# Optimization experiments

Hardware: AMD Instinct MI355X
Metric: run time of the kernel (lower is better)

The kernel has to match this reference:

```python
import jax, jax.numpy as jnp
import numpy as np

B, S, D = 8, 1024, 1024

def setup_inputs() -> dict:
    key = jax.random.key(0)
    ks = jax.random.split(key, 6)
    context = jax.random.normal(ks[0], (B, S, D), dtype=jnp.float32)
    eos_mask = jax.random.randint(ks[1], (B, S), 0, 2, dtype=jnp.int32)
    prior = jax.random.uniform(ks[2], (), dtype=jnp.float32)
    adj_mat = jax.random.randint(ks[3], (B, S, S), 0, 2, dtype=jnp.int32)
    Wk = jax.random.normal(ks[4], (D, D), dtype=jnp.float32) * 0.02
    Wq = jax.random.normal(ks[5], (D, D), dtype=jnp.float32) * 0.02
    bk = jnp.zeros((D,), jnp.float32)
    bq = jnp.zeros((D,), jnp.float32)
    ln_gamma = jnp.ones((D,), jnp.float32)
    ln_beta = jnp.zeros((D,), jnp.float32)
    return {"context": context, "eos_mask": eos_mask, "prior": prior,
            "adj_mat": adj_mat, "Wk": Wk, "bk": bk, "Wq": Wq, "bq": bq,
            "ln_gamma": ln_gamma, "ln_beta": ln_beta}

def reference(context, eos_mask, prior, adj_mat, Wk, bk, Wq, bq, ln_gamma, ln_beta):
    d_model = context.shape[-1]
    seq_len = context.shape[1]
    # LayerNorm (annotated-transformer style: unbiased std, eps added to std)
    mu = jnp.mean(context, axis=-1, keepdims=True)
    std = jnp.std(context, axis=-1, keepdims=True, ddof=1)
    x = ln_gamma * (context - mu) / (std + 1e-6) + ln_beta
    # projections (torch Linear: x @ W.T + b)
    key_p = x @ Wk.T + bk
    query = x @ Wq.T + bq
    scores = jnp.einsum('bqd,bkd->bqk', query, key_p) / (d_model / 2)
    scores = jnp.where(adj_mat == 0, -1e9, scores)
    neibor_attn = jax.nn.softmax(scores, axis=-1)
    neibor_attn = jnp.sqrt(neibor_attn * jnp.swapaxes(neibor_attn, -1, -2) + 1e-9)
    neibor_attn = prior + (1.0 - prior) * neibor_attn
    # constant structural matrices
    a = jnp.eye(seq_len, k=1, dtype=jnp.float32)          # superdiagonal
    b = jnp.eye(seq_len, dtype=jnp.float32)               # diagonal
    tri = jnp.triu(jnp.ones((seq_len, seq_len), jnp.float32))  # upper incl diag
    # t = (log(attn+eps) masked to superdiagonal) @ tri
    t = jnp.matmul(jnp.where(a == 0, 0.0, jnp.log(neibor_attn + 1e-9)), tri)
    g_attn = jnp.exp(jnp.matmul(tri, t))
    g_attn = jnp.where((tri - b) == 0, 0.0, g_attn)  # keep strict upper only
    g_attn = g_attn + jnp.swapaxes(g_attn, -1, -2) + jnp.where(b == 0, 1e-9, neibor_attn)
    return (g_attn, neibor_attn)
```

## Files before the change

kernel.cpp:

```cpp
#include <hip/hip_runtime.h>
#include <hip/hip_bf16.h>

#define S_LEN 1024
#define D_DIM 1024
#define N_BAT 8
#define BSS   (8ull*1024ull*1024ull)

using bf16x8 = __attribute__((ext_vector_type(8))) short;
using f32x4  = __attribute__((ext_vector_type(4))) float;

__device__ __forceinline__ short f2bf(float v) {
    __hip_bfloat16 h = __float2bfloat16(v);
    return *reinterpret_cast<short*>(&h);
}

__device__ __forceinline__ void gload_lds16(const void* g, void* l) {
    __builtin_amdgcn_global_load_lds(
        (const __attribute__((address_space(1))) void*)g,
        (__attribute__((address_space(3))) void*)l, 16, 0, 0);
}

__device__ __forceinline__ int xcd_remap_flat() {
    const int nwg  = gridDim.x * gridDim.y * gridDim.z;
    const int flat = blockIdx.x + gridDim.x * (blockIdx.y + gridDim.y * blockIdx.z);
    const int cpx  = nwg >> 3;
    return (flat & 7) * cpx + (flat >> 3);
}

__device__ __forceinline__ void gemm_mainloop(
    const short* __restrict__ A, const short* __restrict__ Bt,
    int brow, int bcol, short* As, short* Bs, f32x4 acc[4][4])
{
    const int tid  = threadIdx.x;
    const int lane = tid & 63;
    const int w    = tid >> 6;
    const int wr   = w >> 1, wc = w & 1;
    const int q0   = w * 4096 + lane * 16;
    const int rsel = lane & 15;
    const int kb   = (lane >> 4) * 16;

#pragma unroll
    for (int m = 0; m < 4; ++m)
#pragma unroll
        for (int n = 0; n < 4; ++n) acc[m][n] = 0.0f;

#pragma unroll
    for (int c = 0; c < 4; ++c) {
        const int q    = q0 + c * 1024;
        const int row  = q >> 7;
        const int colb = (q & 127) ^ ((row & 7) << 4);
        gload_lds16((const char*)(A  + (size_t)(brow + row) * 1024) + colb,
                    (char*)As + q);
        gload_lds16((const char*)(Bt + (size_t)(bcol + row) * 1024) + colb,
                    (char*)Bs + q);
    }
    __syncthreads();

    for (int t = 0; t < 16; ++t) {
        const int cur = t & 1;
        const char* Ac = (const char*)As + cur * 16384;
        const char* Bc = (const char*)Bs + cur * 16384;
        if (t < 15) {
            const int k0 = (t + 1) * 64;
            char* An = (char*)As + (cur ^ 1) * 16384;
            char* Bn = (char*)Bs + (cur ^ 1) * 16384;
#pragma unroll
            for (int c = 0; c < 4; ++c) {
                const int q    = q0 + c * 1024;
                const int row  = q >> 7;
                const int colb = (q & 127) ^ ((row & 7) << 4);
                gload_lds16((const char*)(A  + (size_t)(brow + row) * 1024 + k0) + colb,
                            An + q);
                gload_lds16((const char*)(Bt + (size_t)(bcol + row) * 1024 + k0) + colb,
                            Bn + q);
            }
        }
        bf16x8 af[4][2], bfr[4][2];
#pragma unroll
        for (int m = 0; m < 4; ++m) {
            const int row = wr * 64 + m * 16 + rsel;
            const int sw  = (row & 7) << 4;
#pragma unroll
            for (int kk = 0; kk < 2; ++kk)
                af[m][kk] = *(const bf16x8*)&Ac[row * 128 + ((kk * 64 + kb) ^ sw)];
        }
#pragma unroll
        for (int n = 0; n < 4; ++n) {
            const int row = wc * 64 + n * 16 + rsel;
            const int sw  = (row & 7) << 4;
#pragma unroll
            for (int kk = 0; kk < 2; ++kk)
                bfr[n][kk] = *(const bf16x8*)&Bc[row * 128 + ((kk * 64 + kb) ^ sw)];
        }
#pragma unroll
        for (int kk = 0; kk < 2; ++kk)
#pragma unroll
            for (int m = 0; m < 4; ++m)
#pragma unroll
                for (int n = 0; n < 4; ++n)
                    acc[m][n] = __builtin_amdgcn_mfma_f32_16x16x32_bf16(
                        af[m][kk], bfr[n][kk], acc[m][n], 0, 0, 0);
        __syncthreads();
    }
}

__global__ __launch_bounds__(256) void gemm_bf16(
    const short* __restrict__ A, const short* __restrict__ Bt,
    short* __restrict__ C)
{
    __shared__ short As[2 * 8192];
    __shared__ short Bs[2 * 8192];
    const int nid = xcd_remap_flat();
    const int mx  = nid % gridDim.x;
    const int ny  = nid / gridDim.x;
    const int brow = mx * 128, bcol = ny * 128;

    f32x4 acc[4][4];
    gemm_mainloop(A, Bt, brow, bcol, As, Bs, acc);

    const int lane = threadIdx.x & 63;
    const int w    = threadIdx.x >> 6;
    const int wr   = w >> 1, wc = w & 1;
#pragma unroll
    for (int m = 0; m < 4; ++m)
#pragma unroll
        for (int n = 0; n < 4; ++n) {
            const int colg = bcol + wc * 64 + n * 16 + (lane & 15);
#pragma unroll
            for (int r = 0; r < 4; ++r) {
                const int rowg = brow + wr * 64 + m * 16 + ((lane >> 4) * 4 + r);
                C[(size_t)rowg * 1024 + colg] = f2bf(acc[m][n][r]);
            }
        }
}

__global__ __launch_bounds__(256) void gemm_scores(
    const short* __restrict__ Tm, const short* __restrict__ Xm,
    const float* __restrict__ p, const float* __restrict__ r2,
    const float* __restrict__ c0p, float* __restrict__ Sc)
{
    __shared__ short As[2 * 8192];
    __shared__ short Bs[2 * 8192];
    const int nid = xcd_remap_flat();
    const int mx  = nid & 7;
    const int ny  = (nid >> 3) & 7;
    const int b   = nid >> 6;
    const short* A  = Tm + (size_t)b * 1024 * 1024;
    const short* Bt = Xm + (size_t)b * 1024 * 1024;
    const float* pb = p  + (size_t)b * 1024;
    const float* rb = r2 + (size_t)b * 1024;
    float* C = Sc + (size_t)b * 1024 * 1024;
    const int brow = mx * 128, bcol = ny * 128;

    f32x4 acc[4][4];
    gemm_mainloop(A, Bt, brow, bcol, As, Bs, acc);

    const int lane = threadIdx.x & 63;
    const int w    = threadIdx.x >> 6;
    const int wr   = w >> 1, wc = w & 1;
    const float c0v = c0p[0];
#pragma unroll
    for (int m = 0; m < 4; ++m)
#pragma unroll
        for (int n = 0; n < 4; ++n) {
            const int colg = bcol + wc * 64 + n * 16 + (lane & 15);
            const float radd = rb[colg] + c0v;
#pragma unroll
            for (int r = 0; r < 4; ++r) {
                const int rowg = brow + wr * 64 + m * 16 + ((lane >> 4) * 4 + r);
                C[(size_t)rowg * 1024 + colg] =
                    (acc[m][n][r] + pb[rowg] + radd) * 0.001953125f;
            }
        }
}

__global__ __launch_bounds__(256) void bias_gemv1(
    const float* __restrict__ Wq, const float* __restrict__ Wk,
    const float* __restrict__ bk, const float* __restrict__ bq,
    float* __restrict__ pu, float* __restrict__ pv)
{
    __shared__ float su[8][128];
    __shared__ float sv[8][128];
    const int tx = threadIdx.x & 31;
    const int ty = threadIdx.x >> 5;
    const int colBase = blockIdx.x * 128;
    const int rowBase = blockIdx.y * 64;
    const int i = colBase + tx * 4;
    float4 au = {0,0,0,0}, av = {0,0,0,0};
#pragma unroll
    for (int jj = 0; jj < 8; ++jj) {
        const int j = rowBase + ty + jj * 8;
        const float bkv = bk[j], bqv = bq[j];
        const float4 wq = *(const float4*)&Wq[(size_t)j * 1024 + i];
        const float4 wk = *(const float4*)&Wk[(size_t)j * 1024 + i];
        au.x += wq.x * bkv; au.y += wq.y * bkv; au.z += wq.z * bkv; au.w += wq.w * bkv;
        av.x += wk.x * bqv; av.y += wk.y * bqv; av.z += wk.z * bqv; av.w += wk.w * bqv;
    }
    ((float4*)su[ty])[tx] = au;
    ((float4*)sv[ty])[tx] = av;
    __syncthreads();
    if (ty == 0) {
        float4 s1 = ((float4*)su[0])[tx];
        float4 s2 = ((float4*)sv[0])[tx];
#pragma unroll
        for (int k = 1; k < 8; ++k) {
            const float4 t1 = ((float4*)su[k])[tx];
            const float4 t2 = ((float4*)sv[k])[tx];
            s1.x += t1.x; s1.y += t1.y; s1.z += t1.z; s1.w += t1.w;
            s2.x += t2.x; s2.y += t2.y; s2.z += t2.z; s2.w += t2.w;
        }
        ((float4*)&pu[(size_t)blockIdx.y * 1024 + colBase])[tx] = s1;
        ((float4*)&pv[(size_t)blockIdx.y * 1024 + colBase])[tx] = s2;
    }
}

__global__ __launch_bounds__(256) void bias_gemv2(
    const float* __restrict__ pu, const float* __restrict__ pv,
    const float* __restrict__ bk, const float* __restrict__ bq,
    float* __restrict__ u, float* __restrict__ v, float* __restrict__ c0)
{
    __shared__ float sh[4];
    const int i = blockIdx.x * 256 + threadIdx.x;
    float su = 0.0f, sv = 0.0f;
#pragma unroll
    for (int k = 0; k < 16; ++k) {
        su += pu[k * 1024 + i];
        sv += pv[k * 1024 + i];
    }
    u[i] = su;
    v[i] = sv;
    if (blockIdx.x == 0) {
        const int t = threadIdx.x;
        const float4 a = ((const float4*)bq)[t];
        const float4 b = ((const float4*)bk)[t];
        float s = a.x*b.x + a.y*b.y + a.z*b.z + a.w*b.w;
        for (int off = 32; off > 0; off >>= 1) s += __shfl_down(s, off);
        const int lane = t & 63, w = t >> 6;
        if (lane == 0) sh[w] = s;
        __syncthreads();
        if (t == 0) c0[0] = sh[0] + sh[1] + sh[2] + sh[3];
    }
}

__global__ __launch_bounds__(256) void ln_kernel(
    const float* __restrict__ X, const float* __restrict__ gamma,
    const float* __restrict__ beta, const float* __restrict__ u,
    const float* __restrict__ v2, short* __restrict__ Y,
    float* __restrict__ p, float* __restrict__ r2)
{
    __shared__ float sh[16];
    const size_t row = blockIdx.x;
    const int t = threadIdx.x;
    float4 v = ((const float4*)(X + row * 1024))[t];
    float s  = v.x + v.y + v.z + v.w;
    float ss = v.x*v.x + v.y*v.y + v.z*v.z + v.w*v.w;
    for (int off = 32; off > 0; off >>= 1) {
        s  += __shfl_down(s, off);
        ss += __shfl_down(ss, off);
    }
    const int lane = t & 63, w = t >> 6;
    if (lane == 0) { sh[w] = s; sh[4 + w] = ss; }
    __syncthreads();
    if (t == 0) {
        float S  = sh[0] + sh[1] + sh[2] + sh[3];
        float SS = sh[4] + sh[5] + sh[6] + sh[7];
        float mu = S * (1.0f / 1024.0f);
        float var = fmaxf((SS - S * mu) * (1.0f / 1023.0f), 0.0f);
        sh[0] = mu;
        sh[1] = 1.0f / (sqrtf(var) + 1e-6f);
    }
    __syncthreads();
    const float mu = sh[0], inv = sh[1];
    float4 g  = ((const float4*)gamma)[t];
    float4 be = ((const float4*)beta)[t];
    float y0 = g.x * (v.x - mu) * inv + be.x;
    float y1 = g.y * (v.y - mu) * inv + be.y;
    float y2 = g.z * (v.z - mu) * inv + be.z;
    float y3 = g.w * (v.w - mu) * inv + be.w;
    short4 o;
    o.x = f2bf(y0); o.y = f2bf(y1); o.z = f2bf(y2); o.w = f2bf(y3);
    ((short4*)(Y + row * 1024))[t] = o;
    float4 uu = ((const float4*)u)[t];
    float4 vv = ((const float4*)v2)[t];
    float dp = y0*uu.x + y1*uu.y + y2*uu.z + y3*uu.w;
    float dr = y0*vv.x + y1*vv.y + y2*vv.z + y3*vv.w;
    for (int off = 32; off > 0; off >>= 1) {
        dp += __shfl_down(dp, off);
        dr += __shfl_down(dr, off);
    }
    if (lane == 0) { sh[8 + w] = dp; sh[12 + w] = dr; }
    __syncthreads();
    if (t == 0) {
        p[row]  = sh[8] + sh[9] + sh[10] + sh[11];
        r2[row] = sh[12] + sh[13] + sh[14] + sh[15];
    }
}

__global__ __launch_bounds__(256) void cvt_t_kernel(
    const float* __restrict__ Wq, const float* __restrict__ Wk,
    short* __restrict__ wqt, short* __restrict__ wkt)
{
    __shared__ float T[32][33];
    const float* src = blockIdx.z ? Wk : Wq;
    short* dst = blockIdx.z ? wkt : wqt;
    const int bi = blockIdx.x * 32, bj = blockIdx.y * 32;
    const int c = threadIdx.x & 31, r0 = threadIdx.x >> 5;
#pragma unroll
    for (int rr = 0; rr < 4; ++rr) {
        const int r = r0 + rr * 8;
        T[r][c] = src[(size_t)(bi + r) * 1024 + bj + c];
    }
    __syncthreads();
#pragma unroll
    for (int rr = 0; rr < 4; ++rr) {
        const int r = r0 + rr * 8;
        dst[(size_t)(bj + r) * 1024 + bi + c] = f2bf(T[c][r]);
    }
}

__global__ __launch_bounds__(256) void softmax_kernel(
    const float* __restrict__ Sc, const int* __restrict__ adj,
    float* __restrict__ At)
{
    __shared__ float sh[4];
    const size_t row = blockIdx.x;
    const int t = threadIdx.x;
    const float4 sv = ((const float4*)(Sc + row * 1024))[t];
    const int4   av = ((const int4*)(adj + row * 1024))[t];
    float m = -3.0e38f;
    if (av.x) m = fmaxf(m, sv.x);
    if (av.y) m = fmaxf(m, sv.y);
    if (av.z) m = fmaxf(m, sv.z);
    if (av.w) m = fmaxf(m, sv.w);
    for (int off = 32; off > 0; off >>= 1) m = fmaxf(m, __shfl_down(m, off));
    const int lane = t & 63, w = t >> 6;
    if (lane == 0) sh[w] = m;
    __syncthreads();
    const float M = fmaxf(fmaxf(sh[0], sh[1]), fmaxf(sh[2], sh[3]));
    __syncthreads();
    float e0 = av.x ? expf(sv.x - M) : 0.0f;
    float e1 = av.y ? expf(sv.y - M) : 0.0f;
    float e2 = av.z ? expf(sv.z - M) : 0.0f;
    float e3 = av.w ? expf(sv.w - M) : 0.0f;
    float s = e0 + e1 + e2 + e3;
    for (int off = 32; off > 0; off >>= 1) s += __shfl_down(s, off);
    if (lane == 0) sh[w] = s;
    __syncthreads();
    const float Sm = sh[0] + sh[1] + sh[2] + sh[3];
    float4 o;
    if (Sm > 0.0f) {
        const float inv = 1.0f / Sm;
        o.x = e0 * inv; o.y = e1 * inv; o.z = e2 * inv; o.w = e3 * inv;
    } else {
        o.x = o.y = o.z = o.w = 1.0f / 1024.0f;
    }
    ((float4*)(At + row * 1024))[t] = o;
}

__global__ __launch_bounds__(1024) void cum2_kernel(
    const float* __restrict__ At, const float* __restrict__ prior_p,
    double* __restrict__ cum)
{
    __shared__ double sh[1024];
    const int b = blockIdx.x;
    const int t = threadIdx.x;
    const float prior = *prior_p;
    const float om = 1.0f - prior;
    const float* attn = At + (size_t)b * 1024 * 1024;
    double v = 0.0;
    if (t >= 1) {
        const int k = t - 1;
        const float a1 = attn[(size_t)k * 1024 + (k + 1)];
        const float a2 = attn[(size_t)(k + 1) * 1024 + k];
        const float na = prior + om * sqrtf(a1 * a2 + 1e-9f);
        v = (double)logf(na + 1e-9f);
    }
    sh[t] = v;
    __syncthreads();
#pragma unroll
    for (int off = 1; off < 1024; off <<= 1) {
        const double add = (t >= off) ? sh[t - off] : 0.0;
        __syncthreads();
        sh[t] += add;
        __syncthreads();
    }
    cum[b * 1024 + t] = sh[t];
}

__global__ __launch_bounds__(256) void na_g_kernel(
    float* __restrict__ At, const float* __restrict__ prior_p,
    const double* __restrict__ cum, float* __restrict__ G)
{
    const int ti = blockIdx.x >> 5, tj = blockIdx.x & 31;
    if (tj < ti) return;
    const int b = blockIdx.y;
    const float prior = *prior_p;
    const float om = 1.0f - prior;
    float* base = At + (size_t)b * 1024 * 1024;
    float* gb   = G  + (size_t)b * 1024 * 1024;
    const double* cb = cum + (size_t)b * 1024;
    __shared__ float T1[32][33];
    __shared__ float T2[32][33];
    const int c = threadIdx.x & 31, r0 = threadIdx.x >> 5;
#pragma unroll
    for (int rr = 0; rr < 4; ++rr) {
        const int r = r0 + rr * 8;
        T1[r][c] = base[(size_t)(ti * 32 + r) * 1024 + tj * 32 + c];
        T2[r][c] = base[(size_t)(tj * 32 + r) * 1024 + ti * 32 + c];
    }
    __syncthreads();
#pragma unroll
    for (int rr = 0; rr < 4; ++rr) {
        const int r = r0 + rr * 8;
        const int R1 = ti * 32 + r, C1 = tj * 32 + c;
        const float na1 = prior + om * sqrtf(T1[r][c] * T2[c][r] + 1e-9f);
        base[(size_t)R1 * 1024 + C1] = na1;
        float g1;
        if (R1 == C1) g1 = na1;
        else {
            const int lo = min(R1, C1), hi = max(R1, C1);
            g1 = expf((float)(cb[hi] - cb[lo])) + 1e-9f;
        }
        gb[(size_t)R1 * 1024 + C1] = g1;
        const int R2 = tj * 32 + r, C2 = ti * 32 + c;
        const float na2 = prior + om * sqrtf(T2[r][c] * T1[c][r] + 1e-9f);
        base[(size_t)R2 * 1024 + C2] = na2;
        float g2;
        if (R2 == C2) g2 = na2;
        else {
            const int lo = min(R2, C2), hi = max(R2, C2);
            g2 = expf((float)(cb[hi] - cb[lo])) + 1e-9f;
        }
        gb[(size_t)R2 * 1024 + C2] = g2;
    }
}

extern "C" void kernel_launch(void* const* d_in, const int* in_sizes, int n_in,
                              void* d_out, int out_size, void* d_ws, size_t ws_size,
                              hipStream_t stream)
{
    const float* context = (const float*)d_in[0];
    const float* prior   = (const float*)d_in[2];
    const int*   adj     = (const int*)d_in[3];
    const float* Wk      = (const float*)d_in[4];
    const float* bk      = (const float*)d_in[5];
    const float* Wq      = (const float*)d_in[6];
    const float* bq      = (const float*)d_in[7];
    const float* gamma   = (const float*)d_in[8];
    const float* beta    = (const float*)d_in[9];

    float* out   = (float*)d_out;
    float* gout  = out;
    float* naout = out + BSS;

    char* ws = (char*)d_ws;
    short*  xb   = (short*)(ws);
    short*  wqt  = (short*)(ws + (16ull << 20));
    short*  wkt  = (short*)(ws + (18ull << 20));
    short*  m2t  = (short*)(ws + (20ull << 20));
    short*  tb   = (short*)(ws + (22ull << 20));
    double* cumd = (double*)(ws + (38ull << 20));
    float*  uvec = (float*)(ws + (38ull << 20) + (1ull << 16));
    float*  vvec = uvec + 1024;
    float*  c0   = vvec + 1024;
    float*  pvec = c0 + 64;
    float*  rvec = pvec + 8192;
    float*  pu   = rvec + 8192;
    float*  pv   = pu + 16384;

    bias_gemv1<<<dim3(8, 16), 256, 0, stream>>>(Wq, Wk, bk, bq, pu, pv);
    bias_gemv2<<<4, 256, 0, stream>>>(pu, pv, bk, bq, uvec, vvec, c0);
    ln_kernel<<<8192, 256, 0, stream>>>(context, gamma, beta, uvec, vvec,
                                        xb, pvec, rvec);
    cvt_t_kernel<<<dim3(32, 32, 2), 256, 0, stream>>>(Wq, Wk, wqt, wkt);
    gemm_bf16<<<dim3(8, 8), 256, 0, stream>>>(wkt, wqt, m2t);
    gemm_bf16<<<dim3(64, 8), 256, 0, stream>>>(xb, m2t, tb);
    gemm_scores<<<dim3(8, 8, 8), 256, 0, stream>>>(tb, xb, pvec, rvec, c0, gout);
    softmax_kernel<<<8192, 256, 0, stream>>>(gout, adj, naout);
    cum2_kernel<<<8, 1024, 0, stream>>>(naout, prior, cumd);
    na_g_kernel<<<dim3(1024, 8), 256, 0, stream>>>(naout, prior, cumd, gout);
}
```

Baseline: 146.3 us.

## Use 8-wave GEMM blocks and split-K for the weight-product GEMM

Result: faster. 141.2 us (-3.5%).

```diff
diff --git a/kernel.cpp b/kernel.cpp
--- a/kernel.cpp
+++ b/kernel.cpp
@@ -27,55 +27,57 @@
     return (flat & 7) * cpx + (flat >> 3);
 }
 
-__device__ __forceinline__ void gemm_mainloop(
+__device__ __forceinline__ void gemm_mainloop8(
     const short* __restrict__ A, const short* __restrict__ Bt,
-    int brow, int bcol, short* As, short* Bs, f32x4 acc[4][4])
+    int brow, int bcol, int kstart, int kIters,
+    short* As, short* Bs, f32x4 acc[4][2])
 {
     const int tid  = threadIdx.x;
     const int lane = tid & 63;
     const int w    = tid >> 6;
-    const int wr   = w >> 1, wc = w & 1;
-    const int q0   = w * 4096 + lane * 16;
+    const int wr   = w >> 2;
+    const int wc   = w & 3;
     const int rsel = lane & 15;
     const int kb   = (lane >> 4) * 16;
 
+    const int b0   = w * 1024;
+    const int b1   = 8192 + w * 1024;
+    const int ch0  = b0 + lane * 16;
+    const int ch1  = b1 + lane * 16;
+    const int row0 = ch0 >> 7;
+    const int cb0  = (ch0 & 127) ^ ((row0 & 7) << 4);
+    const int row1 = ch1 >> 7;
+    const int cb1  = (ch1 & 127) ^ ((row1 & 7) << 4);
+
 #pragma unroll
     for (int m = 0; m < 4; ++m)
 #pragma unroll
-        for (int n = 0; n < 4; ++n) acc[m][n] = 0.0f;
-
-#pragma unroll
-    for (int c = 0; c < 4; ++c) {
-        const int q    = q0 + c * 1024;
-        const int row  = q >> 7;
-        const int colb = (q & 127) ^ ((row & 7) << 4);
-        gload_lds16((const char*)(A  + (size_t)(brow + row) * 1024) + colb,
-                    (char*)As + q);
-        gload_lds16((const char*)(Bt + (size_t)(bcol + row) * 1024) + colb,
-                    (char*)Bs + q);
-    }
-    __syncthreads();
-
-    for (int t = 0; t < 16; ++t) {
+        for (int n = 0; n < 2; ++n) acc[m][n] = 0.0f;
+
+    {
+        char* Ad = (char*)As;
+        char* Bd = (char*)Bs;
+        gload_lds16((const char*)(A  + (size_t)(brow + row0) * 1024 + kstart) + cb0, Ad + b0);
+        gload_lds16((const char*)(A  + (size_t)(brow + row1) * 1024 + kstart) + cb1, Ad + b1);
+        gload_lds16((const char*)(Bt + (size_t)(bcol + row0) * 1024 + kstart) + cb0, Bd + b0);
+        gload_lds16((const char*)(Bt + (size_t)(bcol + row1) * 1024 + kstart) + cb1, Bd + b1);
+    }
+    __syncthreads();
+
+    for (int t = 0; t < kIters; ++t) {
         const int cur = t & 1;
         const char* Ac = (const char*)As + cur * 16384;
         const char* Bc = (const char*)Bs + cur * 16384;
-        if (t < 15) {
-            const int k0 = (t + 1) * 64;
+        if (t + 1 < kIters) {
+            const int k0 = kstart + (t + 1) * 64;
             char* An = (char*)As + (cur ^ 1) * 16384;
             char* Bn = (char*)Bs + (cur ^ 1) * 16384;
-#pragma unroll
-            for (int c = 0; c < 4; ++c) {
-                const int q    = q0 + c * 1024;
-                const int row  = q >> 7;
-                const int colb = (q & 127) ^ ((row & 7) << 4);
-                gload_lds16((const char*)(A  + (size_t)(brow + row) * 1024 + k0) + colb,
-                            An + q);
-                gload_lds16((const char*)(Bt + (size_t)(bcol + row) * 1024 + k0) + colb,
-                            Bn + q);
-            }
-        }
-        bf16x8 af[4][2], bfr[4][2];
+            gload_lds16((const char*)(A  + (size_t)(brow + row0) * 1024 + k0) + cb0, An + b0);
+            gload_lds16((const char*)(A  + (size_t)(brow + row1) * 1024 + k0) + cb1, An + b1);
+            gload_lds16((const char*)(Bt + (size_t)(bcol + row0) * 1024 + k0) + cb0, Bn + b0);
+            gload_lds16((const char*)(Bt + (size_t)(bcol + row1) * 1024 + k0) + cb1, Bn + b1);
+        }
+        bf16x8 af[4][2], bfr[2][2];
 #pragma unroll
         for (int m = 0; m < 4; ++m) {
             const int row = wr * 64 + m * 16 + rsel;
@@ -85,8 +87,8 @@
                 af[m][kk] = *(const bf16x8*)&Ac[row * 128 + ((kk * 64 + kb) ^ sw)];
         }
 #pragma unroll
-        for (int n = 0; n < 4; ++n) {
-            const int row = wc * 64 + n * 16 + rsel;
+        for (int n = 0; n < 2; ++n) {
+            const int row = wc * 32 + n * 16 + rsel;
             const int sw  = (row & 7) << 4;
 #pragma unroll
             for (int kk = 0; kk < 2; ++kk)
@@ -97,35 +99,35 @@
 #pragma unroll
             for (int m = 0; m < 4; ++m)
 #pragma unroll
-                for (int n = 0; n < 4; ++n)
+                for (int n = 0; n < 2; ++n)
                     acc[m][n] = __builtin_amdgcn_mfma_f32_16x16x32_bf16(
                         af[m][kk], bfr[n][kk], acc[m][n], 0, 0, 0);
         __syncthreads();
     }
 }
 
-__global__ __launch_bounds__(256) void gemm_bf16(
+__global__ __launch_bounds__(512) void gemm_bf16(
     const short* __restrict__ A, const short* __restrict__ Bt,
     short* __restrict__ C)
 {
     __shared__ short As[2 * 8192];
     __shared__ short Bs[2 * 8192];
     const int nid = xcd_remap_flat();
-    const int mx  = nid % gridDim.x;
-    const int ny  = nid / gridDim.x;
+    const int mx  = ((nid >> 6) << 3) + (nid & 7);
+    const int ny  = (nid >> 3) & 7;
     const int brow = mx * 128, bcol = ny * 128;
 
-    f32x4 acc[4][4];
-    gemm_mainloop(A, Bt, brow, bcol, As, Bs, acc);
+    f32x4 acc[4][2];
+    gemm_mainloop8(A, Bt, brow, bcol, 0, 16, As, Bs, acc);
 
     const int lane = threadIdx.x & 63;
     const int w    = threadIdx.x >> 6;
-    const int wr   = w >> 1, wc = w & 1;
+    const int wr   = w >> 2, wc = w & 3;
 #pragma unroll
     for (int m = 0; m < 4; ++m)
 #pragma unroll
-        for (int n = 0; n < 4; ++n) {
-            const int colg = bcol + wc * 64 + n * 16 + (lane & 15);
+        for (int n = 0; n < 2; ++n) {
+            const int colg = bcol + wc * 32 + n * 16 + (lane & 15);
 #pragma unroll
             for (int r = 0; r < 4; ++r) {
                 const int rowg = brow + wr * 64 + m * 16 + ((lane >> 4) * 4 + r);
@@ -134,7 +136,7 @@
         }
 }
 
-__global__ __launch_bounds__(256) void gemm_scores(
+__global__ __launch_bounds__(512) void gemm_scores(
     const short* __restrict__ Tm, const short* __restrict__ Xm,
     const float* __restrict__ p, const float* __restrict__ r2,
     const float* __restrict__ c0p, float* __restrict__ Sc)
@@ -152,18 +154,18 @@
     float* C = Sc + (size_t)b * 1024 * 1024;
     const int brow = mx * 128, bcol = ny * 128;
 
-    f32x4 acc[4][4];
-    gemm_mainloop(A, Bt, brow, bcol, As, Bs, acc);
+    f32x4 acc[4][2];
+    gemm_mainloop8(A, Bt, brow, bcol, 0, 16, As, Bs, acc);
 
     const int lane = threadIdx.x & 63;
     const int w    = threadIdx.x >> 6;
-    const int wr   = w >> 1, wc = w & 1;
+    const int wr   = w >> 2, wc = w & 3;
     const float c0v = c0p[0];
 #pragma unroll
     for (int m = 0; m < 4; ++m)
 #pragma unroll
-        for (int n = 0; n < 4; ++n) {
-            const int colg = bcol + wc * 64 + n * 16 + (lane & 15);
+        for (int n = 0; n < 2; ++n) {
+            const int colg = bcol + wc * 32 + n * 16 + (lane & 15);
             const float radd = rb[colg] + c0v;
 #pragma unroll
             for (int r = 0; r < 4; ++r) {
@@ -172,6 +174,53 @@
                     (acc[m][n][r] + pb[rowg] + radd) * 0.001953125f;
             }
         }
+}
+
+__global__ __launch_bounds__(512) void gemm_splitk(
+    const short* __restrict__ A, const short* __restrict__ Bt,
+    float* __restrict__ P)
+{
+    __shared__ short As[2 * 8192];
+    __shared__ short Bs[2 * 8192];
+    const int brow = blockIdx.x * 128, bcol = blockIdx.y * 128;
+    const int z = blockIdx.z;
+
+    f32x4 acc[4][2];
+    gemm_mainloop8(A, Bt, brow, bcol, z * 256, 4, As, Bs, acc);
+
+    float* Pz = P + (size_t)z * 1024 * 1024;
+    const int lane = threadIdx.x & 63;
+    const int w    = threadIdx.x >> 6;
+    const int wr   = w >> 2, wc = w & 3;
+#pragma unroll
+    for (int m = 0; m < 4; ++m)
+#pragma unroll
+        for (int n = 0; n < 2; ++n) {
+            const int colg = bcol + wc * 32 + n * 16 + (lane & 15);
+#pragma unroll
+            for (int r = 0; r < 4; ++r) {
+                const int rowg = brow + wr * 64 + m * 16 + ((lane >> 4) * 4 + r);
+                Pz[(size_t)rowg * 1024 + colg] = acc[m][n][r];
+            }
+        }
+}
+
+__global__ __launch_bounds__(256) void reduce_m2t(
+    const float* __restrict__ P, short* __restrict__ M)
+{
+    const int idx = blockIdx.x * 256 + threadIdx.x;
+    const float4* P4 = (const float4*)P;
+    float4 s = P4[idx];
+    const float4 s1 = P4[idx + 262144];
+    const float4 s2 = P4[idx + 524288];
+    const float4 s3 = P4[idx + 786432];
+    s.x += s1.x + s2.x + s3.x;
+    s.y += s1.y + s2.y + s3.y;
+    s.z += s1.z + s2.z + s3.z;
+    s.w += s1.w + s2.w + s3.w;
+    short4 o;
+    o.x = f2bf(s.x); o.y = f2bf(s.y); o.z = f2bf(s.z); o.w = f2bf(s.w);
+    ((short4*)M)[idx] = o;
 }
 
 __global__ __launch_bounds__(256) void bias_gemv1(
@@ -454,28 +503,30 @@
     float* naout = out + BSS;
 
     char* ws = (char*)d_ws;
-    short*  xb   = (short*)(ws);
-    short*  wqt  = (short*)(ws + (16ull << 20));
-    short*  wkt  = (short*)(ws + (18ull << 20));
-    short*  m2t  = (short*)(ws + (20ull << 20));
-    short*  tb   = (short*)(ws + (22ull << 20));
-    double* cumd = (double*)(ws + (38ull << 20));
-    float*  uvec = (float*)(ws + (38ull << 20) + (1ull << 16));
-    float*  vvec = uvec + 1024;
-    float*  c0   = vvec + 1024;
-    float*  pvec = c0 + 64;
-    float*  rvec = pvec + 8192;
-    float*  pu   = rvec + 8192;
-    float*  pv   = pu + 16384;
+    short*  xb    = (short*)(ws);
+    short*  wqt   = (short*)(ws + (16ull << 20));
+    short*  wkt   = (short*)(ws + (18ull << 20));
+    short*  m2t   = (short*)(ws + (20ull << 20));
+    short*  tb    = (short*)(ws + (22ull << 20));
+    float*  m2par = (float*)tb;
+    double* cumd  = (double*)(ws + (38ull << 20));
+    float*  uvec  = (float*)(ws + (38ull << 20) + (1ull << 16));
+    float*  vvec  = uvec + 1024;
+    float*  c0    = vvec + 1024;
+    float*  pvec  = c0 + 64;
+    float*  rvec  = pvec + 8192;
+    float*  pu    = rvec + 8192;
+    float*  pv    = pu + 16384;
 
     bias_gemv1<<<dim3(8, 16), 256, 0, stream>>>(Wq, Wk, bk, bq, pu, pv);
     bias_gemv2<<<4, 256, 0, stream>>>(pu, pv, bk, bq, uvec, vvec, c0);
     ln_kernel<<<8192, 256, 0, stream>>>(context, gamma, beta, uvec, vvec,
                                         xb, pvec, rvec);
     cvt_t_kernel<<<dim3(32, 32, 2), 256, 0, stream>>>(Wq, Wk, wqt, wkt);
-    gemm_bf16<<<dim3(8, 8), 256, 0, stream>>>(wkt, wqt, m2t);
-    gemm_bf16<<<dim3(64, 8), 256, 0, stream>>>(xb, m2t, tb);
-    gemm_scores<<<dim3(8, 8, 8), 256, 0, stream>>>(tb, xb, pvec, rvec, c0, gout);
+    gemm_splitk<<<dim3(8, 8, 4), 512, 0, stream>>>(wkt, wqt, m2par);
+    reduce_m2t<<<1024, 256, 0, stream>>>(m2par, m2t);
+    gemm_bf16<<<dim3(64, 8), 512, 0, stream>>>(xb, m2t, tb);
+    gemm_scores<<<dim3(8, 8, 8), 512, 0, stream>>>(tb, xb, pvec, rvec, c0, gout);
     softmax_kernel<<<8192, 256, 0, stream>>>(gout, adj, naout);
     cum2_kernel<<<8, 1024, 0, stream>>>(naout, prior, cumd);
     na_g_kernel<<<dim3(1024, 8), 256, 0, stream>>>(naout, prior, cumd, gout);
```
